# Optimization experiments

Hardware: AMD Instinct MI355X
Metric: run time of the kernel (lower is better)

Reference implementation:

```python
import jax, jax.numpy as jnp
import numpy as np
from jax import lax

H = 32  # hidden_size


def setup_inputs() -> dict:
    key = jax.random.key(0)
    ks = jax.random.split(key, 7)
    B, T, I, O = 4096, 4096, 1, 1
    s = 1.0 / np.sqrt(H)
    return {
        "x": jax.random.normal(ks[0], (B, T, I), dtype=jnp.float32),
        "h_init": jnp.zeros((1, B, H), dtype=jnp.float32),
        "W_ih": jax.random.uniform(ks[1], (H, I), jnp.float32, -s, s),
        "W_hh": jax.random.uniform(ks[2], (H, H), jnp.float32, -s, s),
        "b_ih": jax.random.uniform(ks[3], (H,), jnp.float32, -s, s),
        "b_hh": jax.random.uniform(ks[4], (H,), jnp.float32, -s, s),
        "W_reg": jax.random.uniform(ks[5], (O, H), jnp.float32, -s, s),
        "b_reg": jax.random.uniform(ks[6], (O,), jnp.float32, -s, s),
    }


def reference(x, h_init, W_ih, W_hh, b_ih, b_hh, W_reg, b_reg):
    # Elman RNN with ReLU, batch_first: h_t = relu(x_t W_ih^T + b_ih + h_{t-1} W_hh^T + b_hh)
    # Precompute the input projection for all steps at once: [B,T,H]
    xin = jnp.einsum('bti,hi->bth', x, W_ih) + (b_ih + b_hh)
    xin_t = jnp.moveaxis(xin, 1, 0)  # [T,B,H] for scan over time

    def step(h, xt):  # h: [B,H], xt: [B,H]
        h_new = jax.nn.relu(xt + h @ W_hh.T)
        return h_new, None

    hn, _ = lax.scan(step, h_init[0], xin_t)  # hn: [B,H] (final hidden of layer 0)
    # module reshapes hn to [num_layers*B, H] (num_layers=1) then applies Linear
    return hn @ W_reg.T + b_reg  # [B,1]
```

## Files before the change

### kernel.cpp

```cpp
#include <hip/hip_runtime.h>


#define HSZ 32

typedef _Float16 half8 __attribute__((ext_vector_type(8)));
typedef _Float16 h2n __attribute__((ext_vector_type(2)));
typedef __fp16 fp16x2 __attribute__((ext_vector_type(2)));
typedef float f32x4 __attribute__((ext_vector_type(4)));
typedef float f32x2 __attribute__((ext_vector_type(2)));

static __device__ __forceinline__ fp16x2 relu_pk(fp16x2 a) {
  union {
    fp16x2 r;
    h2n n;
  } u;
  u.r = a;
  h2n z = {(_Float16)0.f, (_Float16)0.f};
  u.n = __builtin_elementwise_max(u.n, z);
  return u.r;
}

__global__ __attribute__((amdgpu_flat_work_group_size(64, 64),
                          amdgpu_waves_per_eu(1, 1)))
void rnn_reg_kernel(
    const float* __restrict__ x, const float* __restrict__ h_init,
    const float* __restrict__ W_ih, const float* __restrict__ W_hh,
    const float* __restrict__ b_ih, const float* __restrict__ b_hh,
    const float* __restrict__ W_reg, const float* __restrict__ b_reg,
    float* __restrict__ out, int T) {
  const int lane = threadIdx.x;
  const int lo4  = lane & 15;
  const int q    = lane >> 4;
  const int bg   = blockIdx.x * 16 + lo4;

  const int u1m = 8 * (lo4 >> 2) + (lo4 & 3);
  half8 A1, A2;
#pragma unroll
  for (int j = 0; j < 8; ++j) {
    A1[j] = (_Float16)W_hh[u1m * HSZ + 8 * q + j];
    A2[j] = (_Float16)W_hh[(u1m + 4) * HSZ + 8 * q + j];
  }

  const int m0 = 8 * q;
  f32x2 wih1a = {W_ih[m0 + 0], W_ih[m0 + 1]};
  f32x2 wih1b = {W_ih[m0 + 2], W_ih[m0 + 3]};
  f32x2 wih2a = {W_ih[m0 + 4], W_ih[m0 + 5]};
  f32x2 wih2b = {W_ih[m0 + 6], W_ih[m0 + 7]};
  f32x2 bia1a = {b_ih[m0 + 0] + b_hh[m0 + 0], b_ih[m0 + 1] + b_hh[m0 + 1]};
  f32x2 bia1b = {b_ih[m0 + 2] + b_hh[m0 + 2], b_ih[m0 + 3] + b_hh[m0 + 3]};
  f32x2 bia2a = {b_ih[m0 + 4] + b_hh[m0 + 4], b_ih[m0 + 5] + b_hh[m0 + 5]};
  f32x2 bia2b = {b_ih[m0 + 6] + b_hh[m0 + 6], b_ih[m0 + 7] + b_hh[m0 + 7]};

  half8 bfrag;
#pragma unroll
  for (int i = 0; i < 8; ++i)
    bfrag[i] = (_Float16)h_init[(size_t)bg * HSZ + 8 * q + i];

  f32x4 d1g = {0.f, 0.f, 0.f, 0.f};
  f32x4 d2g = {0.f, 0.f, 0.f, 0.f};

#define STEP(xv)                                                              \
  do {                                                                        \
    f32x2 xx = {(xv), (xv)};                                                  \
    f32x2 p0 = __builtin_elementwise_fma(wih1a, xx, bia1a);                   \
    f32x2 p1 = __builtin_elementwise_fma(wih1b, xx, bia1b);                   \
    f32x2 p2 = __builtin_elementwise_fma(wih2a, xx, bia2a);                   \
    f32x2 p3 = __builtin_elementwise_fma(wih2b, xx, bia2b);                   \
    f32x4 c1 = __builtin_shufflevector(p0, p1, 0, 1, 2, 3);                   \
    f32x4 c2 = __builtin_shufflevector(p2, p3, 0, 1, 2, 3);                   \
    f32x4 d1 = __builtin_amdgcn_mfma_f32_16x16x32_f16(A1, bfrag, c1, 0, 0, 0);\
    f32x4 d2 = __builtin_amdgcn_mfma_f32_16x16x32_f16(A2, bfrag, c2, 0, 0, 0);\
    d1g = d1;                                                                 \
    d2g = d2;                                                                 \
    union { fp16x2 h2[4]; half8 h8; } cv;                                     \
    cv.h2[0] = relu_pk(__builtin_amdgcn_cvt_pkrtz(d1[0], d1[1])); \
    cv.h2[1] = relu_pk(__builtin_amdgcn_cvt_pkrtz(d1[2], d1[3])); \
    cv.h2[2] = relu_pk(__builtin_amdgcn_cvt_pkrtz(d2[0], d2[1])); \
    cv.h2[3] = relu_pk(__builtin_amdgcn_cvt_pkrtz(d2[2], d2[3])); \
    bfrag = cv.h8;                                                            \
  } while (0)

  const float4* xr = (const float4*)(x + (size_t)bg * (size_t)T);
  const int last = T / 4 - 1;
  float4 xa = xr[0], xb = xr[1];

#pragma unroll 1
  for (int t = 0; t < T; t += 8) {
    int i0 = (t >> 2) + 2; if (i0 > last) i0 = last;
    int i1 = (t >> 2) + 3; if (i1 > last) i1 = last;
    float4 na = xr[i0];
    float4 nb = xr[i1];
    STEP(xa.x); STEP(xa.y); STEP(xa.z); STEP(xa.w);
    STEP(xb.x); STEP(xb.y); STEP(xb.z); STEP(xb.w);
    xa = na; xb = nb;
  }

  float v = 0.f;
#pragma unroll
  for (int r = 0; r < 4; ++r) {
    v = fmaf(fmaxf(d1g[r], 0.f), W_reg[8 * q + r], v);
    v = fmaf(fmaxf(d2g[r], 0.f), W_reg[8 * q + 4 + r], v);
  }
  v += __shfl_xor(v, 16, 64);
  v += __shfl_xor(v, 32, 64);
  if (q == 0) out[bg] = v + b_reg[0];
}

extern "C" void kernel_launch(void* const* d_in, const int* in_sizes, int n_in,
                              void* d_out, int out_size, void* d_ws, size_t ws_size,
                              hipStream_t stream) {
  const float* x      = (const float*)d_in[0];
  const float* h_init = (const float*)d_in[1];
  const float* W_ih   = (const float*)d_in[2];
  const float* W_hh   = (const float*)d_in[3];
  const float* b_ih   = (const float*)d_in[4];
  const float* b_hh   = (const float*)d_in[5];
  const float* W_reg  = (const float*)d_in[6];
  const float* b_reg  = (const float*)d_in[7];
  float* out = (float*)d_out;

  const int B = in_sizes[1] / HSZ;
  const int T = in_sizes[0] / B;
  const int grid = B / 16;

  rnn_reg_kernel<<<dim3(grid), dim3(64), 0, stream>>>(
      x, h_init, W_ih, W_hh, b_ih, b_hh, W_reg, b_reg, out, T);
}
```

Before: 450.7 us.

## Interleave four independent batch chains per wave to hide MFMA latency

```diff
diff --git a/kernel.cpp b/kernel.cpp
--- a/kernel.cpp
+++ b/kernel.cpp
@@ -7,7 +7,6 @@
 typedef _Float16 h2n __attribute__((ext_vector_type(2)));
 typedef __fp16 fp16x2 __attribute__((ext_vector_type(2)));
 typedef float f32x4 __attribute__((ext_vector_type(4)));
-typedef float f32x2 __attribute__((ext_vector_type(2)));
 
 static __device__ __forceinline__ fp16x2 relu_pk(fp16x2 a) {
   union {
@@ -31,7 +30,10 @@
   const int lane = threadIdx.x;
   const int lo4  = lane & 15;
   const int q    = lane >> 4;
-  const int bg   = blockIdx.x * 16 + lo4;
+  const int bg0 = blockIdx.x * 64 + lo4;
+  const int bg1 = bg0 + 16;
+  const int bg2 = bg0 + 32;
+  const int bg3 = bg0 + 48;
 
   const int u1m = 8 * (lo4 >> 2) + (lo4 & 3);
   half8 A1, A2;
@@ -41,69 +43,108 @@
     A2[j] = (_Float16)W_hh[(u1m + 4) * HSZ + 8 * q + j];
   }
 
-  const int m0 = 8 * q;
-  f32x2 wih1a = {W_ih[m0 + 0], W_ih[m0 + 1]};
-  f32x2 wih1b = {W_ih[m0 + 2], W_ih[m0 + 3]};
-  f32x2 wih2a = {W_ih[m0 + 4], W_ih[m0 + 5]};
-  f32x2 wih2b = {W_ih[m0 + 6], W_ih[m0 + 7]};
-  f32x2 bia1a = {b_ih[m0 + 0] + b_hh[m0 + 0], b_ih[m0 + 1] + b_hh[m0 + 1]};
-  f32x2 bia1b = {b_ih[m0 + 2] + b_hh[m0 + 2], b_ih[m0 + 3] + b_hh[m0 + 3]};
-  f32x2 bia2a = {b_ih[m0 + 4] + b_hh[m0 + 4], b_ih[m0 + 5] + b_hh[m0 + 5]};
-  f32x2 bia2b = {b_ih[m0 + 6] + b_hh[m0 + 6], b_ih[m0 + 7] + b_hh[m0 + 7]};
+  float wih[8], bia[8];
+#pragma unroll
+  for (int r = 0; r < 8; ++r) {
+    int m = 8 * q + r;
+    wih[r] = W_ih[m];
+    bia[r] = b_ih[m] + b_hh[m];
+  }
 
-  half8 bfrag;
+  half8 bf0, bf1, bf2, bf3;
 #pragma unroll
-  for (int i = 0; i < 8; ++i)
-    bfrag[i] = (_Float16)h_init[(size_t)bg * HSZ + 8 * q + i];
+  for (int i = 0; i < 8; ++i) {
+    bf0[i] = (_Float16)h_init[(size_t)bg0 * HSZ + 8 * q + i];
+    bf1[i] = (_Float16)h_init[(size_t)bg1 * HSZ + 8 * q + i];
+    bf2[i] = (_Float16)h_init[(size_t)bg2 * HSZ + 8 * q + i];
+    bf3[i] = (_Float16)h_init[(size_t)bg3 * HSZ + 8 * q + i];
+  }
 
-  f32x4 d1g = {0.f, 0.f, 0.f, 0.f};
-  f32x4 d2g = {0.f, 0.f, 0.f, 0.f};
+  f32x4 d1g0, d2g0, d1g1, d2g1, d1g2, d2g2, d1g3, d2g3;
 
-#define STEP(xv)                                                              \
+#define STEP(S, xv)                                                           \
   do {                                                                        \
-    f32x2 xx = {(xv), (xv)};                                                  \
-    f32x2 p0 = __builtin_elementwise_fma(wih1a, xx, bia1a);                   \
-    f32x2 p1 = __builtin_elementwise_fma(wih1b, xx, bia1b);                   \
-    f32x2 p2 = __builtin_elementwise_fma(wih2a, xx, bia2a);                   \
-    f32x2 p3 = __builtin_elementwise_fma(wih2b, xx, bia2b);                   \
-    f32x4 c1 = __builtin_shufflevector(p0, p1, 0, 1, 2, 3);                   \
-    f32x4 c2 = __builtin_shufflevector(p2, p3, 0, 1, 2, 3);                   \
-    f32x4 d1 = __builtin_amdgcn_mfma_f32_16x16x32_f16(A1, bfrag, c1, 0, 0, 0);\
-    f32x4 d2 = __builtin_amdgcn_mfma_f32_16x16x32_f16(A2, bfrag, c2, 0, 0, 0);\
-    d1g = d1;                                                                 \
-    d2g = d2;                                                                 \
+    f32x4 c1, c2;                                                             \
+    c1[0] = fmaf((xv), wih[0], bia[0]); c1[1] = fmaf((xv), wih[1], bia[1]);   \
+    c1[2] = fmaf((xv), wih[2], bia[2]); c1[3] = fmaf((xv), wih[3], bia[3]);   \
+    c2[0] = fmaf((xv), wih[4], bia[4]); c2[1] = fmaf((xv), wih[5], bia[5]);   \
+    c2[2] = fmaf((xv), wih[6], bia[6]); c2[3] = fmaf((xv), wih[7], bia[7]);   \
+    f32x4 d1 = __builtin_amdgcn_mfma_f32_16x16x32_f16(A1, bf##S, c1, 0, 0, 0);\
+    f32x4 d2 = __builtin_amdgcn_mfma_f32_16x16x32_f16(A2, bf##S, c2, 0, 0, 0);\
     union { fp16x2 h2[4]; half8 h8; } cv;                                     \
     cv.h2[0] = relu_pk(__builtin_amdgcn_cvt_pkrtz(d1[0], d1[1])); \
     cv.h2[1] = relu_pk(__builtin_amdgcn_cvt_pkrtz(d1[2], d1[3])); \
     cv.h2[2] = relu_pk(__builtin_amdgcn_cvt_pkrtz(d2[0], d2[1])); \
     cv.h2[3] = relu_pk(__builtin_amdgcn_cvt_pkrtz(d2[2], d2[3])); \
-    bfrag = cv.h8;                                                            \
+    bf##S = cv.h8;                                                            \
   } while (0)
 
-  const float4* xr = (const float4*)(x + (size_t)bg * (size_t)T);
-  const int last = T / 4 - 1;
-  float4 xa = xr[0], xb = xr[1];
+#define STEPD(S, xv)                                                          \
+  do {                                                                        \
+    f32x4 c1, c2;                                                             \
+    c1[0] = fmaf((xv), wih[0], bia[0]); c1[1] = fmaf((xv), wih[1], bia[1]);   \
+    c1[2] = fmaf((xv), wih[2], bia[2]); c1[3] = fmaf((xv), wih[3], bia[3]);   \
+    c2[0] = fmaf((xv), wih[4], bia[4]); c2[1] = fmaf((xv), wih[5], bia[5]);   \
+    c2[2] = fmaf((xv), wih[6], bia[6]); c2[3] = fmaf((xv), wih[7], bia[7]);   \
+    d1g##S = __builtin_amdgcn_mfma_f32_16x16x32_f16(A1, bf##S, c1, 0, 0, 0);  \
+    d2g##S = __builtin_amdgcn_mfma_f32_16x16x32_f16(A2, bf##S, c2, 0, 0, 0);  \
+  } while (0)
+
+#define SS4(BUF, COMP)                                                        \
+  STEP(0, BUF##_0.COMP); STEP(1, BUF##_1.COMP);                               \
+  STEP(2, BUF##_2.COMP); STEP(3, BUF##_3.COMP)
+
+  const float4* xr0 = (const float4*)(x + (size_t)bg0 * (size_t)T);
+  const float4* xr1 = (const float4*)(x + (size_t)bg1 * (size_t)T);
+  const float4* xr2 = (const float4*)(x + (size_t)bg2 * (size_t)T);
+  const float4* xr3 = (const float4*)(x + (size_t)bg3 * (size_t)T);
+
+  float4 q0_0 = xr0[0], q0_1 = xr1[0], q0_2 = xr2[0], q0_3 = xr3[0];
+  float4 q1_0 = xr0[1], q1_1 = xr1[1], q1_2 = xr2[1], q1_3 = xr3[1];
+  float4 q2_0 = xr0[2], q2_1 = xr1[2], q2_2 = xr2[2], q2_3 = xr3[2];
+  float4 q3_0 = xr0[3], q3_1 = xr1[3], q3_2 = xr2[3], q3_3 = xr3[3];
 
 #pragma unroll 1
-  for (int t = 0; t < T; t += 8) {
-    int i0 = (t >> 2) + 2; if (i0 > last) i0 = last;
-    int i1 = (t >> 2) + 3; if (i1 > last) i1 = last;
-    float4 na = xr[i0];
-    float4 nb = xr[i1];
-    STEP(xa.x); STEP(xa.y); STEP(xa.z); STEP(xa.w);
-    STEP(xb.x); STEP(xb.y); STEP(xb.z); STEP(xb.w);
-    xa = na; xb = nb;
+  for (int t = 0; t < T - 16; t += 16) {
+    xr0 += 4; xr1 += 4; xr2 += 4; xr3 += 4;
+    SS4(q0, x); SS4(q0, y); SS4(q0, z); SS4(q0, w);
+    q0_0 = xr0[0]; q0_1 = xr1[0]; q0_2 = xr2[0]; q0_3 = xr3[0];
+    SS4(q1, x); SS4(q1, y); SS4(q1, z); SS4(q1, w);
+    q1_0 = xr0[1]; q1_1 = xr1[1]; q1_2 = xr2[1]; q1_3 = xr3[1];
+    SS4(q2, x); SS4(q2, y); SS4(q2, z); SS4(q2, w);
+    q2_0 = xr0[2]; q2_1 = xr1[2]; q2_2 = xr2[2]; q2_3 = xr3[2];
+    SS4(q3, x); SS4(q3, y); SS4(q3, z); SS4(q3, w);
+    q3_0 = xr0[3]; q3_1 = xr1[3]; q3_2 = xr2[3]; q3_3 = xr3[3];
   }
 
-  float v = 0.f;
+  SS4(q0, x); SS4(q0, y); SS4(q0, z); SS4(q0, w);
+  SS4(q1, x); SS4(q1, y); SS4(q1, z); SS4(q1, w);
+  SS4(q2, x); SS4(q2, y); SS4(q2, z); SS4(q2, w);
+  SS4(q3, x); SS4(q3, y); SS4(q3, z);
+  STEPD(0, q3_0.w); STEPD(1, q3_1.w); STEPD(2, q3_2.w); STEPD(3, q3_3.w);
+
+  float wr[8];
 #pragma unroll
-  for (int r = 0; r < 4; ++r) {
-    v = fmaf(fmaxf(d1g[r], 0.f), W_reg[8 * q + r], v);
-    v = fmaf(fmaxf(d2g[r], 0.f), W_reg[8 * q + 4 + r], v);
-  }
-  v += __shfl_xor(v, 16, 64);
-  v += __shfl_xor(v, 32, 64);
-  if (q == 0) out[bg] = v + b_reg[0];
+  for (int r = 0; r < 8; ++r) wr[r] = W_reg[8 * q + r];
+  const float br = b_reg[0];
+
+#define EPI(S, idx)                                                           \
+  do {                                                                        \
+    float v = 0.f;                                                            \
+    v = fmaf(fmaxf(d1g##S[0], 0.f), wr[0], v);                                \
+    v = fmaf(fmaxf(d1g##S[1], 0.f), wr[1], v);                                \
+    v = fmaf(fmaxf(d1g##S[2], 0.f), wr[2], v);                                \
+    v = fmaf(fmaxf(d1g##S[3], 0.f), wr[3], v);                                \
+    v = fmaf(fmaxf(d2g##S[0], 0.f), wr[4], v);                                \
+    v = fmaf(fmaxf(d2g##S[1], 0.f), wr[5], v);                                \
+    v = fmaf(fmaxf(d2g##S[2], 0.f), wr[6], v);                                \
+    v = fmaf(fmaxf(d2g##S[3], 0.f), wr[7], v);                                \
+    v += __shfl_xor(v, 16, 64);                                               \
+    v += __shfl_xor(v, 32, 64);                                               \
+    if (q == 0) out[idx] = v + br;                                            \
+  } while (0)
+
+  EPI(0, bg0); EPI(1, bg1); EPI(2, bg2); EPI(3, bg3);
 }
 
 extern "C" void kernel_launch(void* const* d_in, const int* in_sizes, int n_in,
@@ -121,7 +162,7 @@
 
   const int B = in_sizes[1] / HSZ;
   const int T = in_sizes[0] / B;
-  const int grid = B / 16;
+  const int grid = B / 64;
 
   rnn_reg_kernel<<<dim3(grid), dim3(64), 0, stream>>>(
       x, h_init, W_ih, W_hh, b_ih, b_hh, W_reg, b_reg, out, T);
```

After: 1.340 ms. +197.3%, slower.
